# Kernel optimization log

Hardware: AMD Instinct MI355X
Metric: run time of the kernel (lower is better)

Reference implementation:

```python
import jax, jax.numpy as jnp
import numpy as np

BITS = 4
GROUP = 128
IN_F = 4096
OUT_F = 11008
N_GROUPS = IN_F // GROUP  # padded_in == in_features here


def fwht(v):
    """Orthonormal fast Walsh-Hadamard transform over the last axis (len = power of 2)."""
    orig = v.shape
    g = orig[-1]
    x = v.reshape(-1, g)
    h = 1
    while h < g:
        x = x.reshape(-1, g // (2 * h), 2, h)
        a, b = x[:, :, 0, :], x[:, :, 1, :]
        x = jnp.stack([a + b, a - b], axis=2).reshape(-1, g)
        h *= 2
    return (x * (1.0 / np.sqrt(g))).reshape(orig)


def setup_inputs() -> dict:
    key = jax.random.key(0)
    ks = jax.random.split(key, 7)
    x = jax.random.normal(ks[0], (4096, IN_F), dtype=jnp.float32)
    # packed 4-bit indices: two per byte, stored as int32 byte values
    packed_weight = jax.random.randint(ks[1], (OUT_F, IN_F // 2), 0, 256, dtype=jnp.int32)
    # per-(row, group) scale factors (positive)
    norms = jax.random.uniform(ks[2], (OUT_F, N_GROUPS), dtype=jnp.float32) * 0.1 + 0.01
    # Lloyd-Max codebook: 2^bits sorted centroids
    centroids = jnp.sort(jax.random.normal(ks[3], (2 ** BITS,), dtype=jnp.float32))
    # Rademacher sign vectors for the two-round signed WHT rotation
    signs1 = jnp.where(jax.random.normal(ks[4], (GROUP,)) >= 0, 1.0, -1.0).astype(jnp.float32)
    signs2 = jnp.where(jax.random.normal(ks[5], (GROUP,)) >= 0, 1.0, -1.0).astype(jnp.float32)
    bias = jax.random.normal(ks[6], (OUT_F,), dtype=jnp.float32) * 0.01
    return {"x": x, "packed_weight": packed_weight, "norms": norms,
            "centroids": centroids, "signs1": signs1, "signs2": signs2, "bias": bias}


def dequantize(packed_weight, norms, centroids, signs1, signs2):
    out_f, n_groups = norms.shape
    # unpack 4-bit nibbles: low nibble at even positions, high nibble at odd
    pw = packed_weight.astype(jnp.uint8)
    lo = (pw & 15).astype(jnp.int32)
    hi = (pw >> 4).astype(jnp.int32)
    idx = jnp.stack([lo, hi], axis=-1).reshape(out_f, -1)      # [out, padded_in]
    c = centroids[idx].reshape(out_f, n_groups, GROUP)          # codebook lookup
    # inverse of rotate(v) = H(s2 * H(s1 * v)):  v = s1 * H(s2 * H(u))
    u = fwht(c) * signs2
    u = fwht(u) * signs1
    w = u * norms[:, :, None]                                   # per-group rescale
    return w.reshape(out_f, -1)


def reference(x, packed_weight, norms, centroids, signs1, signs2, bias):
    w = dequantize(packed_weight, norms, centroids, signs1, signs2)[:, : x.shape[-1]]
    return x @ w.T + bias
```

## Files before the change

kernel.cpp:

```cpp
#include <hip/hip_runtime.h>
#include <stdint.h>

#define M_DIM 4096
#define K_DIM 4096
#define N_DIM 11008
#define N_GROUPS 32

typedef __attribute__((ext_vector_type(8))) short short8;
typedef __attribute__((ext_vector_type(4))) float floatx4;

__device__ __forceinline__ unsigned short f32_to_bf16(float f) {
    unsigned int u = __float_as_uint(f);
    unsigned int rounding = 0x7FFFu + ((u >> 16) & 1u);
    return (unsigned short)((u + rounding) >> 16);
}

__global__ __launch_bounds__(128) void make_M_kernel(
    const float* __restrict__ signs1, const float* __restrict__ signs2,
    unsigned short* __restrict__ Mt)
{
    const int i = blockIdx.x;
    const int j = threadIdx.x;
    __shared__ float s2s[128];
    s2s[j] = signs2[j];
    __syncthreads();
    float acc = 0.f;
#pragma unroll 8
    for (int a = 0; a < 128; ++a) {
        int par = (__popc(i & a) + __popc(a & j)) & 1;
        acc += par ? -s2s[a] : s2s[a];
    }
    Mt[i * 128 + j] = f32_to_bf16(signs1[j] * acc * (1.0f / 128.0f));
}

#define TX_RS 136

__global__ __launch_bounds__(256) void transform_x_kernel(
    const float* __restrict__ x,
    const unsigned short* __restrict__ Mt,
    unsigned short* __restrict__ z)
{
    __shared__ __align__(16) short Xs[64 * TX_RS];
    __shared__ __align__(16) short Ms[128 * TX_RS];

    const int tid = threadIdx.x;
    const int wave = tid >> 6, lane = tid & 63;
    const int col16 = lane & 15, quad = lane >> 4;
    const int m0 = (blockIdx.x >> 5) * 64;
    const int g = blockIdx.x & 31;
    const int c0 = g * 128;

#pragma unroll
    for (int it = 0; it < 8; ++it) {
        int idx = tid + 256 * it;
        int row = idx >> 5, c4 = idx & 31;
        float4 v = *(const float4*)(x + (size_t)(m0 + row) * K_DIM + c0 + c4 * 4);
        uint2 o;
        o.x = (unsigned)f32_to_bf16(v.x) | ((unsigned)f32_to_bf16(v.y) << 16);
        o.y = (unsigned)f32_to_bf16(v.z) | ((unsigned)f32_to_bf16(v.w) << 16);
        *(uint2*)(Xs + row * TX_RS + c4 * 4) = o;
    }
#pragma unroll
    for (int it = 0; it < 8; ++it) {
        int ch = tid + 256 * it;
        int row = ch >> 4, cc = ch & 15;
        uint4 v = *(const uint4*)(Mt + (size_t)ch * 8);
        *(uint4*)(Ms + row * TX_RS + cc * 8) = v;
    }
    __syncthreads();

    floatx4 acc[8] = {};
#pragma unroll
    for (int ks = 0; ks < 4; ++ks) {
        short8 af = *(const short8*)(Xs + (wave * 16 + col16) * TX_RS + ks * 32 + quad * 8);
#pragma unroll
        for (int ni = 0; ni < 8; ++ni) {
            short8 bf = *(const short8*)(Ms + (ni * 16 + col16) * TX_RS + ks * 32 + quad * 8);
            acc[ni] = __builtin_amdgcn_mfma_f32_16x16x32_bf16(af, bf, acc[ni], 0, 0, 0);
        }
    }
#pragma unroll
    for (int ni = 0; ni < 8; ++ni)
#pragma unroll
        for (int r = 0; r < 4; ++r) {
            int row = m0 + wave * 16 + quad * 4 + r;
            z[(size_t)row * K_DIM + c0 + ni * 16 + col16] = f32_to_bf16(acc[ni][r]);
        }
}

__global__ __launch_bounds__(256) void dequant_lut_kernel(
    const int* __restrict__ packed,
    const float* __restrict__ norms,
    const float* __restrict__ centroids,
    unsigned int* __restrict__ w_out)
{
    __shared__ float2 lut[256];
    const int tid = threadIdx.x;
    lut[tid] = make_float2(centroids[tid & 15], centroids[tid >> 4]);
    __syncthreads();

    const int row = blockIdx.x;
    const int g = tid >> 3;
    const float nrm = norms[row * N_GROUPS + g];
    const int* prow = packed + (size_t)row * 2048 + tid * 8;
    int4 pa = *(const int4*)(prow);
    int4 pb = *(const int4*)(prow + 4);
    int v[8] = {pa.x, pa.y, pa.z, pa.w, pb.x, pb.y, pb.z, pb.w};
    unsigned o[8];
#pragma unroll
    for (int q = 0; q < 8; ++q) {
        float2 c = lut[v[q] & 255];
        o[q] = (unsigned)f32_to_bf16(c.x * nrm) | ((unsigned)f32_to_bf16(c.y * nrm) << 16);
    }
    unsigned* orow = w_out + (size_t)row * 2048 + tid * 8;
    *(uint4*)(orow)     = make_uint4(o[0], o[1], o[2], o[3]);
    *(uint4*)(orow + 4) = make_uint4(o[4], o[5], o[6], o[7]);
}

#define BM 256
#define BN 256
#define BK 64

typedef const __attribute__((address_space(1))) void* gvp_t;
typedef __attribute__((address_space(3))) void* svp_t;

#define GFENCE() asm volatile("" ::: "memory")
#define BARRIER() do { GFENCE(); __builtin_amdgcn_s_barrier(); GFENCE(); } while (0)
#define LGKM0() asm volatile("s_waitcnt lgkmcnt(0)" ::: "memory")
#define LGKM8() asm volatile("s_waitcnt lgkmcnt(8)" ::: "memory")
#define VM6()   asm volatile("s_waitcnt vmcnt(6)" ::: "memory")
#define VM4()   asm volatile("s_waitcnt vmcnt(4)" ::: "memory")
#define VM0()   asm volatile("s_waitcnt vmcnt(0)" ::: "memory")
#define PRIO1() __builtin_amdgcn_s_setprio(1)
#define PRIO0() __builtin_amdgcn_s_setprio(0)

__device__ __forceinline__ void read_a4(short8 (&dst)[4][2], const short* rb, int s0) {
#pragma unroll
    for (int fm = 0; fm < 4; ++fm) {
        dst[fm][0] = *(const short8*)(rb + fm * 1024 + s0);
        dst[fm][1] = *(const short8*)(rb + fm * 1024 + (s0 ^ 32));
    }
}
__device__ __forceinline__ void read_b2(short8 (&dst)[2][2], const short* rb, int s0) {
#pragma unroll
    for (int fn = 0; fn < 2; ++fn) {
        dst[fn][0] = *(const short8*)(rb + fn * 1024 + s0);
        dst[fn][1] = *(const short8*)(rb + fn * 1024 + (s0 ^ 32));
    }
}
__device__ __forceinline__ void mfma_q(floatx4 (&acc)[4][2],
                                       const short8 (&a)[4][2], const short8 (&b)[2][2]) {
#pragma unroll
    for (int ks = 0; ks < 2; ++ks)
#pragma unroll
        for (int fm = 0; fm < 4; ++fm)
#pragma unroll
            for (int fn = 0; fn < 2; ++fn)
                acc[fm][fn] = __builtin_amdgcn_mfma_f32_16x16x32_bf16(
                    a[fm][ks], b[fn][ks], acc[fm][fn], 0, 0, 0);
}

__global__ __launch_bounds__(512, 2) void gemm_bt_kernel(
    const unsigned short* __restrict__ A,
    const unsigned short* __restrict__ B,
    const float* __restrict__ bias,
    float* __restrict__ C)
{
    __shared__ __align__(16) short smem[65536];
    short* As = smem;
    short* Bs = smem + 32768;

    const int tid = threadIdx.x;
    const int w = tid >> 6, lane = tid & 63;
    const int wm = w >> 2, wn = w & 3;
    const int col16 = lane & 15, quad = lane >> 4;

    const int bid = blockIdx.x;
    const int xcd = bid & 7, idx = bid >> 3;
    const int mt = xcd * 2 + (idx & 1);
    const int nt = idx >> 1;
    const int m0 = mt * BM, n0 = nt * BN;

    const int gc = (lane & 7) ^ (lane >> 3);
    const unsigned short* aSrc = A + (size_t)(m0 + w * 8 + (lane >> 3)) * K_DIM + gc * 8;
    const unsigned short* bSrc = B + (size_t)(n0 + (w >> 2) * 64 + (w & 3) * 8 + (lane >> 3)) * K_DIM + gc * 8;
    const int wOff = w * 512;

#define STAGE_A(BUF, H, KT) do { \
    __builtin_amdgcn_global_load_lds((gvp_t)(aSrc + (size_t)((H) * 64) * K_DIM + (KT) * 64), \
        (svp_t)(As + (BUF) * 16384 + (H) * 8192 + wOff), 16, 0, 0); \
    __builtin_amdgcn_global_load_lds((gvp_t)(aSrc + (size_t)((H) * 64 + 128) * K_DIM + (KT) * 64), \
        (svp_t)(As + (BUF) * 16384 + (H) * 8192 + 4096 + wOff), 16, 0, 0); \
} while (0)
#define STAGE_B(BUF, H, KT) do { \
    __builtin_amdgcn_global_load_lds((gvp_t)(bSrc + (size_t)((H) * 32) * K_DIM + (KT) * 64), \
        (svp_t)(Bs + (BUF) * 16384 + (H) * 8192 + wOff), 16, 0, 0); \
    __builtin_amdgcn_global_load_lds((gvp_t)(bSrc + (size_t)((H) * 32 + 128) * K_DIM + (KT) * 64), \
        (svp_t)(Bs + (BUF) * 16384 + (H) * 8192 + 4096 + wOff), 16, 0, 0); \
} while (0)

    const short* aR = As + (wm * 64 + col16) * 64;
    const short* bR = Bs + (wn * 32 + col16) * 64;
    const int s0 = (quad ^ (col16 & 7)) << 3;

    short8 a0[4][2], a1[4][2], b0[2][2], b1[2][2];
    floatx4 acc[2][2][4][2];
#pragma unroll
    for (int i0 = 0; i0 < 2; ++i0)
#pragma unroll
        for (int i1 = 0; i1 < 2; ++i1)
#pragma unroll
            for (int i2 = 0; i2 < 4; ++i2)
#pragma unroll
                for (int i3 = 0; i3 < 2; ++i3)
                    acc[i0][i1][i2][i3] = (floatx4)0.0f;

    STAGE_A(0, 0, 0); STAGE_B(0, 0, 0); STAGE_A(0, 1, 0); STAGE_B(0, 1, 0);
    VM4();
    STAGE_A(1, 0, 1); STAGE_B(1, 0, 1); STAGE_A(1, 1, 1);
    VM6();
    BARRIER();

    const int NIT = K_DIM / (2 * BK) - 1;
    for (int i = 0; i < NIT; ++i) {
        const int t = 2 * i;
        read_a4(a0, aR, s0); read_b2(b0, bR, s0);
        STAGE_B(1, 1, t + 1);
        LGKM8();
        BARRIER(); LGKM0();
        PRIO1(); mfma_q(acc[0][0], a0, b0); PRIO0();
        BARRIER();
        read_a4(a1, aR + 8192, s0);
        STAGE_A(0, 0, t + 2);
        BARRIER(); LGKM0();
        PRIO1(); mfma_q(acc[1][0], a1, b0); PRIO0();
        BARRIER();
        read_b2(b1, bR + 8192, s0);
        STAGE_B(0, 0, t + 2);
        BARRIER(); LGKM0();
        PRIO1(); mfma_q(acc[0][1], a0, b1); PRIO0();
        BARRIER();
        STAGE_A(0, 1, t + 2);
        VM6();
        BARRIER();
        PRIO1(); mfma_q(acc[1][1], a1, b1); PRIO0();
        BARRIER();
        read_a4(a0, aR + 16384, s0); read_b2(b0, bR + 16384, s0);
        STAGE_B(0, 1, t + 2);
        LGKM8();
        BARRIER(); LGKM0();
        PRIO1(); mfma_q(acc[0][0], a0, b0); PRIO0();
        BARRIER();
        read_a4(a1, aR + 16384 + 8192, s0);
        STAGE_A(1, 0, t + 3);
        BARRIER(); LGKM0();
        PRIO1(); mfma_q(acc[1][0], a1, b0); PRIO0();
        BARRIER();
        read_b2(b1, bR + 16384 + 8192, s0);
        STAGE_B(1, 0, t + 3);
        BARRIER(); LGKM0();
        PRIO1(); mfma_q(acc[0][1], a0, b1); PRIO0();
        BARRIER();
        STAGE_A(1, 1, t + 3);
        VM6();
        BARRIER();
        PRIO1(); mfma_q(acc[1][1], a1, b1); PRIO0();
        BARRIER();
    }

    read_a4(a0, aR, s0); read_b2(b0, bR, s0);
    STAGE_B(1, 1, 63);
    BARRIER(); LGKM0();
    mfma_q(acc[0][0], a0, b0);
    BARRIER();
    read_a4(a1, aR + 8192, s0);
    BARRIER(); LGKM0();
    mfma_q(acc[1][0], a1, b0);
    BARRIER();
    read_b2(b1, bR + 8192, s0);
    BARRIER(); LGKM0();
    mfma_q(acc[0][1], a0, b1);
    BARRIER();
    VM0();
    BARRIER();
    mfma_q(acc[1][1], a1, b1);
    read_a4(a0, aR + 16384, s0); read_b2(b0, bR + 16384, s0);
    mfma_q(acc[0][0], a0, b0);
    read_a4(a1, aR + 16384 + 8192, s0);
    mfma_q(acc[1][0], a1, b0);
    read_b2(b1, bR + 16384 + 8192, s0);
    mfma_q(acc[0][1], a0, b1);
    mfma_q(acc[1][1], a1, b1);

#undef STAGE_A
#undef STAGE_B

    float bv[2][2];
#pragma unroll
    for (int qn = 0; qn < 2; ++qn)
#pragma unroll
        for (int fn = 0; fn < 2; ++fn)
            bv[qn][fn] = bias[n0 + wn * 64 + qn * 32 + fn * 16 + col16];

#pragma unroll
    for (int qm = 0; qm < 2; ++qm)
#pragma unroll
        for (int fm = 0; fm < 4; ++fm)
#pragma unroll
            for (int r = 0; r < 4; ++r) {
                float* crow = C + (size_t)(m0 + wm * 128 + qm * 64 + fm * 16 + quad * 4 + r) * N_DIM
                              + n0 + wn * 64 + col16;
#pragma unroll
                for (int qn = 0; qn < 2; ++qn)
#pragma unroll
                    for (int fn = 0; fn < 2; ++fn)
                        crow[qn * 32 + fn * 16] = acc[qm][qn][fm][fn][r] + bv[qn][fn];
            }
}

extern "C" void kernel_launch(void* const* d_in, const int* in_sizes, int n_in,
                              void* d_out, int out_size, void* d_ws, size_t ws_size,
                              hipStream_t stream) {
    const float* x        = (const float*)d_in[0];
    const int* packed     = (const int*)d_in[1];
    const float* norms    = (const float*)d_in[2];
    const float* centroids= (const float*)d_in[3];
    const float* signs1   = (const float*)d_in[4];
    const float* signs2   = (const float*)d_in[5];
    const float* bias     = (const float*)d_in[6];
    float* out            = (float*)d_out;

    unsigned short* Mt     = (unsigned short*)d_ws;
    unsigned short* w_bf16 = (unsigned short*)((char*)d_ws + 32768);
    unsigned short* z_bf16 = (unsigned short*)((char*)d_ws + 32768 + (size_t)N_DIM * K_DIM * 2);

    make_M_kernel<<<128, 128, 0, stream>>>(signs1, signs2, Mt);

    transform_x_kernel<<<(M_DIM / 64) * N_GROUPS, 256, 0, stream>>>(x, Mt, z_bf16);

    dequant_lut_kernel<<<N_DIM, 256, 0, stream>>>(
        packed, norms, centroids, (unsigned int*)w_bf16);

    gemm_bt_kernel<<<dim3((M_DIM / BM) * (N_DIM / BN)), 512, 0, stream>>>(
        z_bf16, w_bf16, bias, out);
}
```

Before: 600.0 us.

## Software-pipeline LDS fragment reads one step ahead of MFMA and drop XCD tile swizzle

Restructures the GEMM main loop so each LDS fragment read is issued before the MFMA block that uses the previous fragments. This removes the explicit lgkmcnt waits and about half the barriers per step, and uses vmcnt(8) gating for the global-to-LDS stages. The intent is to hide LDS latency behind matrix math and cut synchronisation overhead. It also replaces the XCD-aware block-to-tile mapping with a plain row-major mapping, which may change L2 locality. Correctness now depends on the compiler inserting LDS waits and on the reduced barrier count still ordering buffer reuse.

```diff
diff --git a/kernel.cpp b/kernel.cpp
--- a/kernel.cpp
+++ b/kernel.cpp
@@ -124,12 +124,11 @@
 typedef const __attribute__((address_space(1))) void* gvp_t;
 typedef __attribute__((address_space(3))) void* svp_t;
 
-#define GFENCE() asm volatile("" ::: "memory")
-#define BARRIER() do { GFENCE(); __builtin_amdgcn_s_barrier(); GFENCE(); } while (0)
-#define LGKM0() asm volatile("s_waitcnt lgkmcnt(0)" ::: "memory")
-#define LGKM8() asm volatile("s_waitcnt lgkmcnt(8)" ::: "memory")
-#define VM6()   asm volatile("s_waitcnt vmcnt(6)" ::: "memory")
+#define BARRIER() do { asm volatile("" ::: "memory"); __builtin_amdgcn_s_barrier(); \
+                       asm volatile("" ::: "memory"); } while (0)
+#define VM8()   asm volatile("s_waitcnt vmcnt(8)" ::: "memory")
 #define VM4()   asm volatile("s_waitcnt vmcnt(4)" ::: "memory")
+#define VM2()   asm volatile("s_waitcnt vmcnt(2)" ::: "memory")
 #define VM0()   asm volatile("s_waitcnt vmcnt(0)" ::: "memory")
 #define PRIO1() __builtin_amdgcn_s_setprio(1)
 #define PRIO0() __builtin_amdgcn_s_setprio(0)
@@ -176,9 +175,8 @@
     const int col16 = lane & 15, quad = lane >> 4;
 
     const int bid = blockIdx.x;
-    const int xcd = bid & 7, idx = bid >> 3;
-    const int mt = xcd * 2 + (idx & 1);
-    const int nt = idx >> 1;
+    const int mt = bid & 15;
+    const int nt = bid >> 4;
     const int m0 = mt * BM, n0 = nt * BN;
 
     const int gc = (lane & 7) ^ (lane >> 3);
@@ -215,80 +213,72 @@
                 for (int i3 = 0; i3 < 2; ++i3)
                     acc[i0][i1][i2][i3] = (floatx4)0.0f;
 
-    STAGE_A(0, 0, 0); STAGE_B(0, 0, 0); STAGE_A(0, 1, 0); STAGE_B(0, 1, 0);
-    VM4();
-    STAGE_A(1, 0, 1); STAGE_B(1, 0, 1); STAGE_A(1, 1, 1);
-    VM6();
+
+    STAGE_A(0, 0, 0); STAGE_B(0, 0, 0);
+    STAGE_A(0, 1, 0); STAGE_B(0, 1, 0);
+    STAGE_A(1, 0, 1); STAGE_B(1, 0, 1);
+    VM8();
+    BARRIER();
+    read_a4(a0, aR, s0); read_b2(b0, bR, s0);
+    STAGE_A(1, 1, 1);
+    VM8();
     BARRIER();
 
     const int NIT = K_DIM / (2 * BK) - 1;
     for (int i = 0; i < NIT; ++i) {
         const int t = 2 * i;
+        read_a4(a1, aR + 8192, s0);
+        PRIO1(); mfma_q(acc[0][0], a0, b0); PRIO0();
+        STAGE_B(1, 1, t + 1);
+        VM8(); BARRIER();
+        read_b2(b1, bR + 8192, s0);
+        PRIO1(); mfma_q(acc[1][0], a1, b0); PRIO0();
+        STAGE_A(0, 0, t + 2);
+        BARRIER();
+        PRIO1(); mfma_q(acc[0][1], a0, b1); PRIO0();
+        STAGE_B(0, 0, t + 2);
+        VM8(); BARRIER();
+        read_a4(a0, aR + 16384, s0); read_b2(b0, bR + 16384, s0);
+        PRIO1(); mfma_q(acc[1][1], a1, b1); PRIO0();
+        STAGE_A(0, 1, t + 2);
+        VM8(); BARRIER();
+        read_a4(a1, aR + 16384 + 8192, s0);
+        PRIO1(); mfma_q(acc[0][0], a0, b0); PRIO0();
+        STAGE_B(0, 1, t + 2);
+        VM8(); BARRIER();
+        read_b2(b1, bR + 16384 + 8192, s0);
+        PRIO1(); mfma_q(acc[1][0], a1, b0); PRIO0();
+        STAGE_A(1, 0, t + 3);
+        BARRIER();
+        PRIO1(); mfma_q(acc[0][1], a0, b1); PRIO0();
+        STAGE_B(1, 0, t + 3);
+        VM8(); BARRIER();
         read_a4(a0, aR, s0); read_b2(b0, bR, s0);
-        STAGE_B(1, 1, t + 1);
-        LGKM8();
-        BARRIER(); LGKM0();
-        PRIO1(); mfma_q(acc[0][0], a0, b0); PRIO0();
-        BARRIER();
-        read_a4(a1, aR + 8192, s0);
-        STAGE_A(0, 0, t + 2);
-        BARRIER(); LGKM0();
-        PRIO1(); mfma_q(acc[1][0], a1, b0); PRIO0();
-        BARRIER();
-        read_b2(b1, bR + 8192, s0);
-        STAGE_B(0, 0, t + 2);
-        BARRIER(); LGKM0();
-        PRIO1(); mfma_q(acc[0][1], a0, b1); PRIO0();
-        BARRIER();
-        STAGE_A(0, 1, t + 2);
-        VM6();
-        BARRIER();
         PRIO1(); mfma_q(acc[1][1], a1, b1); PRIO0();
-        BARRIER();
-        read_a4(a0, aR + 16384, s0); read_b2(b0, bR + 16384, s0);
-        STAGE_B(0, 1, t + 2);
-        LGKM8();
-        BARRIER(); LGKM0();
-        PRIO1(); mfma_q(acc[0][0], a0, b0); PRIO0();
-        BARRIER();
-        read_a4(a1, aR + 16384 + 8192, s0);
-        STAGE_A(1, 0, t + 3);
-        BARRIER(); LGKM0();
-        PRIO1(); mfma_q(acc[1][0], a1, b0); PRIO0();
-        BARRIER();
-        read_b2(b1, bR + 16384 + 8192, s0);
-        STAGE_B(1, 0, t + 3);
-        BARRIER(); LGKM0();
-        PRIO1(); mfma_q(acc[0][1], a0, b1); PRIO0();
-        BARRIER();
         STAGE_A(1, 1, t + 3);
-        VM6();
-        BARRIER();
-        PRIO1(); mfma_q(acc[1][1], a1, b1); PRIO0();
-        BARRIER();
-    }
-
-    read_a4(a0, aR, s0); read_b2(b0, bR, s0);
+        VM8(); BARRIER();
+    }
+
+    read_a4(a1, aR + 8192, s0);
+    mfma_q(acc[0][0], a0, b0);
     STAGE_B(1, 1, 63);
-    BARRIER(); LGKM0();
+    VM8();
+    BARRIER();
+    read_b2(b1, bR + 8192, s0);
+    mfma_q(acc[1][0], a1, b0);
+    VM4();
+    BARRIER();
+    mfma_q(acc[0][1], a0, b1);
+    VM2();
+    BARRIER();
+    read_a4(a0, aR + 16384, s0); read_b2(b0, bR + 16384, s0);
+    mfma_q(acc[1][1], a1, b1);
+    VM0();
+    BARRIER();
+    read_a4(a1, aR + 16384 + 8192, s0);
     mfma_q(acc[0][0], a0, b0);
-    BARRIER();
-    read_a4(a1, aR + 8192, s0);
-    BARRIER(); LGKM0();
+    read_b2(b1, bR + 16384 + 8192, s0);
     mfma_q(acc[1][0], a1, b0);
-    BARRIER();
-    read_b2(b1, bR + 8192, s0);
-    BARRIER(); LGKM0();
-    mfma_q(acc[0][1], a0, b1);
-    BARRIER();
-    VM0();
-    BARRIER();
-    mfma_q(acc[1][1], a1, b1);
-    read_a4(a0, aR + 16384, s0); read_b2(b0, bR + 16384, s0);
-    mfma_q(acc[0][0], a0, b0);
-    read_a4(a1, aR + 16384 + 8192, s0);
-    mfma_q(acc[1][0], a1, b0);
-    read_b2(b1, bR + 16384 + 8192, s0);
     mfma_q(acc[0][1], a0, b1);
     mfma_q(acc[1][1], a1, b1);
 
```

Result: no change. 593.8 us (-1.0%).
